# Kernel tuning notes

Hardware: AMD Instinct MI355X
Metric: run time of the kernel (lower is better)

## Reference

```python
import jax, jax.numpy as jnp
import numpy as np
from jax import lax

M = 384   # latent_seq_length (match states); insert states = M+1; K = 2M+1
A = 21    # alphabet_length
B = 64    # batch
L = 256   # max observed sequence length
NEG = -1.0e32  # pyro uses -1/epsilon with epsilon=1e-32 for impossible transitions


def _state_indices(Mloc):
    # state k = m + M*g: match states (g=0) m in 0..M-1, insert states (g=1) m in 0..M
    m_k = np.concatenate([np.arange(Mloc), np.arange(Mloc + 1)]).astype(np.int32)
    g_k = np.concatenate([np.zeros(Mloc, np.int32), np.ones(Mloc + 1, np.int32)])
    s_k = (m_k + 1 - g_k).astype(np.int32)  # next decision position, in 0..M
    return m_k, g_k, s_k


def _arrange(precursor_seq_logits, insert_seq_logits, insert_logits, delete_logits):
    """Profile(M) state arranger: assemble initial/transition/emission logits of the
    MuE profile HMM from insertion (r) and deletion (u) log-simplex params.
    insert_logits[m,j] = [log(1-r_mj), log(r_mj)], same for delete/u. Boundary
    convention r_M=1, u_M=0. Vectorized (gathers + cumsum of the delete chain)
    instead of pyro's dense (M,3,2,K,K) transfer einsum -- same math."""
    Mloc = precursor_seq_logits.shape[0]
    dt = precursor_seq_logits.dtype
    m_k, g_k, s_k = _state_indices(Mloc)
    pad_r = jnp.tile(jnp.array([[[NEG, 0.0]]], dt), (1, 3, 1))  # r_M = 1
    pad_u = jnp.tile(jnp.array([[[0.0, NEG]]], dt), (1, 3, 1))  # u_M = 0
    lre = jnp.concatenate([insert_logits, pad_r], 0)  # (M+1,3,2)
    lue = jnp.concatenate([delete_logits, pad_u], 0)  # (M+1,3,2)
    # delete-chain log prob per skipped position j (enter-and-leave delete, type j=2)
    d2 = insert_logits[:, 2, 0] + delete_logits[:, 2, 1]  # (M,)
    C = jnp.concatenate([jnp.zeros((1,), dt), jnp.cumsum(d2), jnp.zeros((1,), dt)])  # C[j]=sum_{i<j} d2[i]
    # per-source-state factors (K,)
    src_stay = lre[s_k, g_k, 0]   # log(1-r_{s,g})
    src_del = lue[s_k, g_k, 1]    # log u_{s,g}
    src_match = lue[s_k, g_k, 0]  # log(1-u_{s,g})
    src_ins = lre[s_k, g_k, 1]    # log r_{s,g}
    # per-target-state factors (K,)
    t_match = lre[m_k, 2, 0] + lue[m_k, 2, 0]
    t_ins = lre[m_k, 2, 1]
    is_ins = g_k == 1
    t_term = jnp.where(is_ins, t_ins, t_match)
    # transition matrix (K,K): direct step, delete-chain step, or impossible
    chain = (src_stay + src_del - C[s_k + 1])[:, None] + C[m_k][None, :]
    same = m_k[None, :] == s_k[:, None]
    fwdm = m_k[None, :] > s_k[:, None]
    direct = jnp.where(is_ins[None, :], src_ins[:, None], (src_stay + src_match)[:, None])
    trans = jnp.where(same, direct, jnp.where(fwdm, chain + t_term[None, :], NEG))
    # initial vector: virtual source (m=-1, g=0) -> s=0 with j=0 params
    i_direct = jnp.where(is_ins, lre[0, 0, 1], lre[0, 0, 0] + lue[0, 0, 0])
    i_chain = lre[0, 0, 0] + lue[0, 0, 1] - C[1] + C[m_k]
    init = jnp.where(m_k == 0, i_direct, i_chain + t_term)
    # emission logits: match states emit precursor, insert states emit insert_seq
    obs = jnp.concatenate([precursor_seq_logits, insert_seq_logits], 0)  # (K,A)
    return init, trans, obs


def _forward(precursor_seq, insert_seq, insert, delete, seq_data, local_scale):
    # log-softmax normalizations done in ProfileHMM.model
    p = precursor_seq - jax.nn.logsumexp(precursor_seq, -1, keepdims=True)
    iseq = insert_seq - jax.nn.logsumexp(insert_seq, -1, keepdims=True)
    r = insert - jax.nn.logsumexp(insert, -1, keepdims=True)
    u = delete - jax.nn.logsumexp(delete, -1, keepdims=True)
    init, trans, obs = _arrange(p, iseq, r, u)
    # MissingDataDiscreteHMM normalizes all logits
    init = init - jax.nn.logsumexp(init)
    trans = trans - jax.nn.logsumexp(trans, -1, keepdims=True)
    obs = obs - jax.nn.logsumexp(obs, -1, keepdims=True)
    # per-position per-state emission log-prob; all-zero rows (missing) give 0
    vl = jnp.einsum('bla,ka->blk', seq_data, obs)  # (B,L,K)
    alpha = init[None, :] + vl[:, 0]               # (B,K)
    Tprob = jnp.exp(trans)                         # (K,K)

    def step(a, vlt):
        # logsumexp_k(a[b,k] + trans[k,kp]) via stable exp-matmul-log
        mx = jnp.max(a, -1, keepdims=True)
        pr = jnp.exp(a - mx) @ Tprob
        return jnp.log(jnp.maximum(pr, 1e-30)) + mx + vlt, None

    alpha, _ = lax.scan(step, alpha, jnp.moveaxis(vl[:, 1:], 1, 0))
    return local_scale[0] * jax.nn.logsumexp(alpha, -1)  # (B,) scaled log-probs


def setup_inputs() -> dict:
    key = jax.random.key(0)
    ks = jax.random.split(key, 6)
    precursor_seq = jax.random.normal(ks[0], (M, A), jnp.float32)
    insert_seq = jax.random.normal(ks[1], (M + 1, A), jnp.float32)
    indel_prior = jnp.array([10.0, 0.0], jnp.float32)  # indel_prior_bias=10 -> rare indels
    insert = indel_prior + jax.random.normal(ks[2], (M, 3, 2), jnp.float32)
    delete = indel_prior + jax.random.normal(ks[3], (M, 3, 2), jnp.float32)
    lengths = jax.random.randint(ks[4], (B,), L // 2, L + 1)
    letters = jax.random.randint(ks[5], (B, L), 0, A)
    onehot = jax.nn.one_hot(letters, A, dtype=jnp.float32)
    mask = (jnp.arange(L)[None, :] < lengths[:, None]).astype(jnp.float32)
    seq_data = onehot * mask[:, :, None]  # zero rows past length = missing data
    return {"precursor_seq": precursor_seq, "insert_seq": insert_seq,
            "insert": insert, "delete": delete, "seq_data": seq_data,
            "local_scale": jnp.ones((1,), jnp.float32)}


def reference(precursor_seq, insert_seq, insert, delete, seq_data, local_scale):
    return _forward(precursor_seq, insert_seq, insert, delete, seq_data, local_scale)
```

## Files before the change

### kernel.cpp

```cpp
#include <hip/hip_runtime.h>


#define NEGC (-1.0e32f)

typedef float v2f __attribute__((ext_vector_type(2)));

#if __has_builtin(__builtin_elementwise_fma)
#define VFMA(a,b,c) __builtin_elementwise_fma((a),(b),(c))
#else
static __device__ __forceinline__ v2f VFMA(v2f a, v2f b, v2f c) {
    v2f r; r.x = fmaf(a.x,b.x,c.x); r.y = fmaf(a.y,b.y,c.y); return r;
}
#endif
#if __has_builtin(__builtin_elementwise_max)
#define VMAX(a,b) __builtin_elementwise_max((a),(b))
#else
static __device__ __forceinline__ v2f VMAX(v2f a, v2f b) {
    v2f r; r.x = fmaxf(a.x,b.x); r.y = fmaxf(a.y,b.y); return r;
}
#endif
static __device__ __forceinline__ v2f mkv2(float a, float b) { v2f r; r.x = a; r.y = b; return r; }

#if __has_builtin(__builtin_amdgcn_sched_barrier)
#define SCHED_FENCE() __builtin_amdgcn_sched_barrier(0x401)
#else
#define SCHED_FENCE()
#endif

template<int CTRL>
__device__ __forceinline__ float fdpp(float x) {
    union { float f; int i; } u, r;
    u.f = x;
    r.i = __builtin_amdgcn_update_dpp(0, u.i, CTRL, 0xF, 0xF, true);
    return r.f;
}
__device__ __forceinline__ float wsr1(float x) { return fdpp<0x138>(x); }

#define L_TAB   0
#define L_ES    16128
#define L_LETS  16152
#define L_TOTAL 16224

#define S_RN    0
#define S_UN    2304
#define S_EWS   4608
#define S_ETMM  4993
#define S_ETII  5378
#define S_CS    5763
#define S_QA    6148
#define S_D2    6533
#define S_AEM   6917
#define S_AEI   7302
#define S_DMA   7687
#define S_DMB   8072
#define S_DIA   8457
#define S_DIB   8842
#define S_RAW   9227
#define S_RED   9998

struct Buf { v2f em0, em1, em2, ei0, ei1, ei2; float es; };

#define RENORM do { \
    v2f mv_ = VMAX(VMAX(Pm0,Pm1), VMAX(Pm2, VMAX(Pi0, VMAX(Pi1,Pi2)))); \
    float mxr_ = fmaxf(fmaxf(mv_.x, mv_.y), pi384); \
    mxr_ = fmaxf(mxr_, fdpp<0x111>(mxr_)); \
    mxr_ = fmaxf(mxr_, fdpp<0x112>(mxr_)); \
    mxr_ = fmaxf(mxr_, fdpp<0x114>(mxr_)); \
    mxr_ = fmaxf(mxr_, fdpp<0x118>(mxr_)); \
    mxr_ = fmaxf(mxr_, fdpp<0x142>(mxr_)); \
    mxr_ = fmaxf(mxr_, fdpp<0x143>(mxr_)); \
    union { float f; int i; } ub_; ub_.f = mxr_; \
    int bits_ = __builtin_amdgcn_readlane(ub_.i, 63); \
    int E_ = (bits_ >> 23) & 0xff; \
    E_ = (E_ < 71) ? 71 : E_; \
    ksum += 197 - E_; \
    union { int i; float f; } us_; us_.i = (324 - E_) << 23; \
    float sc_ = us_.f; \
    Pm0 *= sc_; Pm1 *= sc_; Pm2 *= sc_; Pi0 *= sc_; Pi1 *= sc_; Pi2 *= sc_; pi384 *= sc_; \
} while (0)

#define FILL(LM, E) do { \
    int lmv_ = (LM); \
    int lmc_ = lmv_ > 20 ? 20 : lmv_; \
    const float* bp_ = smem + lmc_*768 + lane12; \
    float4 q0_ = ((const float4*)bp_)[0], q1_ = ((const float4*)bp_)[1], q2_ = ((const float4*)bp_)[2]; \
    E.em0 = mkv2(q0_.x,q0_.y); E.em1 = mkv2(q0_.z,q0_.w); E.em2 = mkv2(q1_.x,q1_.y); \
    E.ei0 = mkv2(q1_.z,q1_.w); E.ei1 = mkv2(q2_.x,q2_.y); E.ei2 = mkv2(q2_.z,q2_.w); \
    E.es = smem[L_ES + lmv_]; \
} while (0)

#define CORE(CUR, FAST) do { \
    float apx_ = wsr1(Pm2.y); \
    float oldPm_ = Pm2.y; \
    v2f Ap0_ = mkv2(apx_, Pm0.x), Ap1_ = mkv2(Pm0.y, Pm1.x), Ap2_ = mkv2(Pm1.y, Pm2.x); \
    v2f E0_ = VFMA(Pi0, Cei0, Ap0_*Cem0); \
    v2f E1_ = VFMA(Pi1, Cei1, Ap1_*Cem1); \
    v2f E2_ = VFMA(Pi2, Cei2, Ap2_*Cem2); \
    float i0_ = E0_.x; \
    float i1_ = fmaf(w1, i0_, E0_.y); \
    float i2_ = fmaf(w2, i1_, E1_.x); \
    float i3_ = fmaf(w3, i2_, E1_.y); \
    float i4_ = fmaf(w4, i3_, E2_.x); \
    float i5_ = fmaf(w5, i4_, E2_.y); \
    float bb_, bx_; \
    if (FAST) { \
        float u_ = wsr1(i5_); \
        bb_ = fmaf(Ar0, u_, i5_);              \
        bx_ = fmaf(Ar0s, wsr1(u_), u_);        \
    } else { \
        bb_ = i5_; \
        bb_ = fmaf(Ar0, fdpp<0x111>(bb_), bb_); \
        bb_ = fmaf(Ar1, fdpp<0x112>(bb_), bb_); \
        bb_ = fmaf(Ar2, fdpp<0x114>(bb_), bb_); \
        bb_ = fmaf(Ar3, fdpp<0x118>(bb_), bb_); \
        bb_ = fmaf(A15, fdpp<0x142>(bb_), bb_); \
        bb_ = fmaf(A31, fdpp<0x143>(bb_), bb_); \
        bx_ = wsr1(bb_); \
    } \
    v2f Rv0_ = mkv2(bx_, fmaf(pw1, bx_, i0_)); \
    v2f Rv1_ = mkv2(fmaf(pw2, bx_, i1_), fmaf(pw3, bx_, i2_)); \
    v2f Rv2_ = mkv2(fmaf(pw4, bx_, i3_), fmaf(pw5, bx_, i4_)); \
    v2f nm0_ = VFMA(Cgm0, Rv0_, VFMA(Pi0, Cdmb0, Ap0_*Cdma0)); \
    v2f nm1_ = VFMA(Cgm1, Rv1_, VFMA(Pi1, Cdmb1, Ap1_*Cdma1)); \
    v2f nm2_ = VFMA(Cgm2, Rv2_, VFMA(Pi2, Cdmb2, Ap2_*Cdma2)); \
    v2f ni0_ = VFMA(Cgi0, Rv0_, VFMA(Pi0, Cdib0, Ap0_*Cdia0)); \
    v2f ni1_ = VFMA(Cgi1, Rv1_, VFMA(Pi1, Cdib1, Ap1_*Cdia1)); \
    v2f ni2_ = VFMA(Cgi2, Rv2_, VFMA(Pi2, Cdib2, Ap2_*Cdia2)); \
    float np_ = ((oldPm_ + pi384) + bb_) * CUR.es;  \
    Pm0 = nm0_*CUR.em0; Pm1 = nm1_*CUR.em1; Pm2 = nm2_*CUR.em2; \
    Pi0 = ni0_*CUR.ei0; Pi1 = ni1_*CUR.ei1; Pi2 = ni2_*CUR.ei2; \
    pi384 = np_; \
} while (0)

#define ITER(BA,BB,BC,LA,LB,LC,TIDX,FAST) do { \
    FILL(LA, BC); \
    LA = (int)lets[(TIDX)+5]; \
    CORE(BA, FAST); \
    SCHED_FENCE(); \
} while (0)

#define SCANLOOP(FAST) do { \
    for (int it = 0; it < bodies; ++it, t += 12) { \
        ITER(bA,bB,bC,lA,lB,lC,t,FAST); \
        ITER(bB,bC,bA,lB,lC,lA,t+1,FAST); \
        ITER(bC,bA,bB,lC,lA,lB,t+2,FAST); \
        ITER(bA,bB,bC,lA,lB,lC,t+3,FAST); \
        ITER(bB,bC,bA,lB,lC,lA,t+4,FAST); \
        ITER(bC,bA,bB,lC,lA,lB,t+5,FAST); \
        ITER(bA,bB,bC,lA,lB,lC,t+6,FAST); \
        ITER(bB,bC,bA,lB,lC,lA,t+7,FAST); \
        ITER(bC,bA,bB,lC,lA,lB,t+8,FAST); \
        ITER(bA,bB,bC,lA,lB,lC,t+9,FAST); \
        ITER(bB,bC,bA,lB,lC,lA,t+10,FAST); \
        ITER(bC,bA,bB,lC,lA,lB,t+11,FAST); \
        RENORM; \
    } \
    if (rem > 0)  { ITER(bA,bB,bC,lA,lB,lC,t,FAST); ++t; } \
    if (rem > 1)  { ITER(bB,bC,bA,lB,lC,lA,t,FAST); ++t; } \
    if (rem > 2)  { ITER(bC,bA,bB,lC,lA,lB,t,FAST); ++t; } \
    if (rem > 3)  { ITER(bA,bB,bC,lA,lB,lC,t,FAST); ++t; } \
    if (rem > 4)  { ITER(bB,bC,bA,lB,lC,lA,t,FAST); ++t; } \
    if (rem > 5)  { ITER(bC,bA,bB,lC,lA,lB,t,FAST); ++t; } \
    if (rem > 6)  { ITER(bA,bB,bC,lA,lB,lC,t,FAST); ++t; } \
    if (rem > 7)  { ITER(bB,bC,bA,lB,lC,lA,t,FAST); ++t; } \
    if (rem > 8)  { ITER(bC,bA,bB,lC,lA,lB,t,FAST); ++t; } \
    if (rem > 9)  { ITER(bA,bB,bC,lA,lB,lC,t,FAST); ++t; } \
    if (rem > 10) { ITER(bB,bC,bA,lB,lC,lA,t,FAST); ++t; } \
} while (0)

__global__ __launch_bounds__(256, 1) void hmm_fused(
    const float* __restrict__ ps, const float* __restrict__ iseq,
    const float* __restrict__ rr, const float* __restrict__ uu,
    const float* __restrict__ seq, const float* __restrict__ lsc,
    float* __restrict__ out)
{
    __shared__ float smem[L_TOTAL];
    const int tid = threadIdx.x;
    const int lane = tid & 63;
    const int wvid = tid >> 6;
    const int b = blockIdx.x;
    unsigned char* lets = (unsigned char*)(smem + L_LETS);

    float* rn   = smem + S_RN;
    float* un   = smem + S_UN;
    float* ews  = smem + S_EWS;
    float* etmm = smem + S_ETMM;
    float* etii = smem + S_ETII;
    float* Cs   = smem + S_CS;
    float* qa   = smem + S_QA;
    float* d2s  = smem + S_D2;
    float* cAEM = smem + S_AEM;
    float* cAEI = smem + S_AEI;
    float* cDMA = smem + S_DMA;
    float* cDMB = smem + S_DMB;
    float* cDIA = smem + S_DIA;
    float* cDIB = smem + S_DIB;
    float* rawv = smem + S_RAW;
    float* red  = smem + S_RED;

    {
        const float* p = seq + (size_t)b*5376 + tid*21;
        float s = 0.f, wsum = 0.f;
        #pragma unroll
        for (int a = 0; a < 21; ++a) { float v = p[a]; s += v; wsum += v*(float)a; }
        lets[tid] = (s > 0.5f) ? (unsigned char)(int)(wsum + 0.5f) : (unsigned char)21;
        if (tid < 8) lets[256 + tid] = (unsigned char)21;
    }
    for (int row = tid; row < 1152; row += 256) {
        float a = rr[row*2], c = rr[row*2+1];
        float mx = fmaxf(a, c);
        float l = mx + __logf(__expf(a-mx) + __expf(c-mx));
        rn[row*2] = a - l; rn[row*2+1] = c - l;
        a = uu[row*2]; c = uu[row*2+1];
        mx = fmaxf(a, c);
        l = mx + __logf(__expf(a-mx) + __expf(c-mx));
        un[row*2] = a - l; un[row*2+1] = c - l;
    }
    __syncthreads();
    for (int m = tid; m < 384; m += 256) {
        float d = rn[(m*3+2)*2+0] + un[(m*3+2)*2+1];
        d2s[m] = d;
        ews[m] = __expf(d);
        etmm[m] = __expf(rn[(m*3+2)*2+0] + un[(m*3+2)*2+0]);
        etii[m] = __expf(rn[(m*3+2)*2+1]);
    }
    if (tid == 0) { ews[384] = 0.f; etmm[384] = 0.f; etii[384] = 1.f; }
    __syncthreads();
    if (tid < 64) {
        float incl[6]; float z = 0.f;
        #pragma unroll
        for (int i = 0; i < 6; ++i) { z += d2s[lane*6+i]; incl[i] = z; }
        float tot = z;
        #pragma unroll
        for (int d = 1; d < 64; d <<= 1) { float q = __shfl_up(tot, d); if (lane >= d) tot += q; }
        float excl = __shfl_up(tot, 1); if (lane == 0) excl = 0.f;
        #pragma unroll
        for (int i = 0; i < 6; ++i) Cs[lane*6+i+1] = excl + incl[i];
        if (lane == 0) Cs[0] = 0.f;
    } else if (tid < 128) {
        float wv6[6], xv[6], incl[6];
        #pragma unroll
        for (int i = 0; i < 6; ++i) {
            int s = 384 - (lane*6 + i);
            wv6[i] = ews[s]; xv[i] = etii[s] + etmm[s];
        }
        float z = 0.f, Wl = 1.f;
        #pragma unroll
        for (int i = 0; i < 6; ++i) { z = fmaf(wv6[i], z, xv[i]); incl[i] = z; Wl *= wv6[i]; }
        float val = z, wt = Wl;
        #pragma unroll
        for (int d = 1; d < 64; d <<= 1) {
            float pv = __shfl_up(val, d); float pwv = __shfl_up(wt, d);
            if (lane >= d) { val = fmaf(wt, pv, val); wt *= pwv; }
        }
        float excl = __shfl_up(val, 1); if (lane == 0) excl = 0.f;
        float pp = 1.f;
        #pragma unroll
        for (int i = 0; i < 6; ++i) {
            pp *= wv6[i];
            qa[383 - (lane*6 + i)] = fmaf(excl, pp, incl[i]);
        }
        if (lane == 0) qa[384] = 0.f;
    }
    __syncthreads();
    for (int k = tid; k < 769; k += 256) {
        int g = (k < 384) ? 0 : 1;
        int m = (k < 384) ? k : (k - 384);
        int s = m + 1 - g;
        float ss, sd, smv, si;
        if (s <= 383) {
            int base = (s*3 + g)*2;
            ss = rn[base+0]; si = rn[base+1];
            smv = un[base+0]; sd = un[base+1];
        } else { ss = NEGC; si = 0.f; smv = 0.f; sd = NEGC; }
        float d0 = (s <= 383) ? (ss + smv) : NEGC;
        float d1 = si;
        float q = qa[s];
        float lq = (q > 0.f) ? __logf(q) : -1.0e30f;
        float ch = ss + sd + lq;
        float mx = fmaxf(fmaxf(d0, d1), ch);
        float Z = mx + __logf(__expf(d0-mx) + __expf(d1-mx) + __expf(ch-mx));
        float we = __expf(ss + sd - Z);
        float w0 = __expf(d0 - Z);
        float w1v = __expf(d1 - Z);
        if (g == 0) { cAEM[s] = we; cDMA[s] = w0; cDIA[s] = w1v; }
        else        { cAEI[s] = we; cDMB[s] = w0; cDIB[s] = w1v; }
    }
    if (tid == 0) { cAEM[0] = 0.f; cDMA[0] = 0.f; cDIA[0] = 0.f; }
    {
        float r000 = rn[0], r001 = rn[1];
        float u000 = un[0], u001 = un[1];
        for (int k = tid; k < 769; k += 256) {
            int g = (k < 384) ? 0 : 1;
            int m = (k < 384) ? k : (k - 384);
            float v;
            if (m == 0) v = g ? r001 : (r000 + u000);
            else {
                float tt = g ? ((m <= 383) ? rn[(m*3+2)*2+1] : 0.f)
                             : (rn[(m*3+2)*2+0] + un[(m*3+2)*2+0]);
                v = r000 + u001 - Cs[1] + Cs[m] + tt;
            }
            rawv[k] = v;
        }
    }
    __syncthreads();
    {
        float lmax = -3.0e38f;
        for (int k = tid; k < 769; k += 256) lmax = fmaxf(lmax, rawv[k]);
        #pragma unroll
        for (int d = 1; d < 64; d <<= 1) lmax = fmaxf(lmax, __shfl_xor(lmax, d));
        if (lane == 0) red[wvid] = lmax;
    }
    __syncthreads();
    {
        float gmax = fmaxf(fmaxf(red[0], red[1]), fmaxf(red[2], red[3]));
        float lsum = 0.f;
        for (int k = tid; k < 769; k += 256) lsum += __expf(rawv[k] - gmax);
        #pragma unroll
        for (int d = 1; d < 64; d <<= 1) lsum += __shfl_xor(lsum, d);
        if (lane == 0) red[4 + wvid] = lsum;
        __syncthreads();
        float lse = gmax + __logf(red[4] + red[5] + red[6] + red[7]);
        for (int k = tid; k < 769; k += 256) rawv[k] = __expf(rawv[k] - lse);
    }
    __syncthreads();
    const int j0 = lane*6;
    const int lane12 = lane*12;
    v2f Cem0=mkv2(cAEM[j0],cAEM[j0+1]), Cem1=mkv2(cAEM[j0+2],cAEM[j0+3]), Cem2=mkv2(cAEM[j0+4],cAEM[j0+5]);
    v2f Cei0=mkv2(cAEI[j0],cAEI[j0+1]), Cei1=mkv2(cAEI[j0+2],cAEI[j0+3]), Cei2=mkv2(cAEI[j0+4],cAEI[j0+5]);
    v2f Cdma0=mkv2(cDMA[j0],cDMA[j0+1]), Cdma1=mkv2(cDMA[j0+2],cDMA[j0+3]), Cdma2=mkv2(cDMA[j0+4],cDMA[j0+5]);
    v2f Cdmb0=mkv2(cDMB[j0],cDMB[j0+1]), Cdmb1=mkv2(cDMB[j0+2],cDMB[j0+3]), Cdmb2=mkv2(cDMB[j0+4],cDMB[j0+5]);
    v2f Cdia0=mkv2(cDIA[j0],cDIA[j0+1]), Cdia1=mkv2(cDIA[j0+2],cDIA[j0+3]), Cdia2=mkv2(cDIA[j0+4],cDIA[j0+5]);
    v2f Cdib0=mkv2(cDIB[j0],cDIB[j0+1]), Cdib1=mkv2(cDIB[j0+2],cDIB[j0+3]), Cdib2=mkv2(cDIB[j0+4],cDIB[j0+5]);
    v2f Cgm0=mkv2(etmm[j0],etmm[j0+1]), Cgm1=mkv2(etmm[j0+2],etmm[j0+3]), Cgm2=mkv2(etmm[j0+4],etmm[j0+5]);
    v2f Cgi0=mkv2(etii[j0],etii[j0+1]), Cgi1=mkv2(etii[j0+2],etii[j0+3]), Cgi2=mkv2(etii[j0+4],etii[j0+5]);
    v2f Pm0=mkv2(rawv[j0],rawv[j0+1]), Pm1=mkv2(rawv[j0+2],rawv[j0+3]), Pm2=mkv2(rawv[j0+4],rawv[j0+5]);
    v2f Pi0=mkv2(rawv[384+j0],rawv[384+j0+1]), Pi1=mkv2(rawv[384+j0+2],rawv[384+j0+3]), Pi2=mkv2(rawv[384+j0+4],rawv[384+j0+5]);
    float pi384 = rawv[768];
    const float W0=ews[j0], w1=ews[j0+1], w2=ews[j0+2], w3=ews[j0+3], w4=ews[j0+4], w5=ews[j0+5];
    __syncthreads();
    for (int row = tid; row < 769; row += 256) {
        const float* src = (row < 384) ? (ps + row*21) : (iseq + (row-384)*21);
        float mx = -3.0e38f;
        for (int a = 0; a < 21; ++a) mx = fmaxf(mx, src[a]);
        float sm2 = 0.f;
        for (int a = 0; a < 21; ++a) sm2 += __expf(src[a]-mx);
        float inv = 1.0f / sm2;
        if (row < 768) {
            int j = (row < 384) ? row : (row - 384);
            int slot = (j/6)*12 + ((row < 384) ? 0 : 6) + (j%6);
            float* dst = smem + L_TAB + slot;
            for (int a = 0; a < 21; ++a) dst[a*768] = __expf(src[a]-mx)*inv;
        } else {
            for (int a = 0; a < 21; ++a) smem[L_ES + a] = __expf(src[a]-mx)*inv;
            smem[L_ES + 21] = 1.0f; smem[L_ES + 22] = 1.0f; smem[L_ES + 23] = 1.0f;
        }
    }
    __syncthreads();
    if (wvid != 0) return;

    int n = 0;
    #pragma unroll
    for (int c = 0; c < 4; ++c)
        n += __popcll(__ballot(lets[c*64 + lane] != (unsigned char)21));

    const float pw1 = W0, pw2 = pw1*w1, pw3 = pw2*w2, pw4 = pw3*w3, pw5 = pw4*w4;
    const float W = pw5*w5;
    float p_ = W;
    const float Ar0 = p_;
    const float Ar0s = wsr1(Ar0);
    { float q = __shfl_up(p_, 1); p_ *= q; } const float Ar1 = p_;
    { float q = __shfl_up(p_, 2); p_ *= q; } const float Ar2 = p_;
    { float q = __shfl_up(p_, 4); p_ *= q; } const float Ar3 = p_;
    float prefR = W;
    #pragma unroll
    for (int d = 1; d < 16; d <<= 1) { float q = __shfl_up(prefR, d); if ((lane & 15) >= d) prefR *= q; }
    const int rw = lane >> 4;
    const float A15 = (rw == 1 || rw == 3) ? prefR : 0.f;
    const float s47 = __shfl(prefR, 47);
    const float A31 = (rw == 2) ? prefR : ((rw == 3) ? prefR * s47 : 0.f);
    bool bad = (Ar1 != 0.f) || (Ar2 != 0.f) || (Ar3 != 0.f)
             || ((A15 != 0.f) && ((lane & 15) >= 1))
             || ((A31 != 0.f) && (lane >= 33));
    const bool fastAll = (__ballot(bad) == 0ull);

    int ksum = 0;
    {
        int lm0 = (int)lets[0];
        const float* bp = smem + lm0*768 + lane12;
        float4 q0 = ((const float4*)bp)[0], q1 = ((const float4*)bp)[1], q2 = ((const float4*)bp)[2];
        Pm0 *= mkv2(q0.x,q0.y); Pm1 *= mkv2(q0.z,q0.w); Pm2 *= mkv2(q1.x,q1.y);
        Pi0 *= mkv2(q1.z,q1.w); Pi1 *= mkv2(q2.x,q2.y); Pi2 *= mkv2(q2.z,q2.w);
        pi384 *= smem[L_ES + lm0];
        RENORM;
    }

    Buf bA, bB, bC;
    FILL((int)lets[1], bA);
    FILL((int)lets[2], bB);
    int lA = (int)lets[3], lB = (int)lets[4], lC = (int)lets[5];

    const int total = n - 1;
    const int bodies = total / 12;
    const int rem = total - bodies*12;
    int t = 1;
    if (fastAll) SCANLOOP(1);
    else         SCANLOOP(0);

    v2f sv = Pm0 + Pm1 + Pm2 + Pi0 + Pi1 + Pi2;
    float s = sv.x + sv.y + ((lane == 63) ? pi384 : 0.f);
    s += fdpp<0x111>(s); s += fdpp<0x112>(s); s += fdpp<0x114>(s); s += fdpp<0x118>(s);
    s += fdpp<0x142>(s); s += fdpp<0x143>(s);
    if (lane == 63) out[b] = lsc[0] * (__logf(s) - (float)ksum * 0.69314718055994531f);
}

extern "C" void kernel_launch(void* const* d_in, const int* in_sizes, int n_in,
                              void* d_out, int out_size, void* d_ws, size_t ws_size,
                              hipStream_t stream)
{
    const float* ps   = (const float*)d_in[0];
    const float* iseq = (const float*)d_in[1];
    const float* ins  = (const float*)d_in[2];
    const float* del  = (const float*)d_in[3];
    const float* seq  = (const float*)d_in[4];
    const float* lsc  = (const float*)d_in[5];
    float* out = (float*)d_out;
    hmm_fused<<<64, 256, 0, stream>>>(ps, iseq, ins, del, seq, lsc, out);
}
```

Baseline: 106.1 us.

## Pack letter and end-state emission into one word, deepen emission prefetch, interleave pairs

Precomputes a per-step integer that holds the clamped letter index in its low byte and the end-insert emission, truncated, in its upper bits. Each scan step then needs one LDS load for both instead of a letter byte load plus a dependent emission load. The emission buffers rotate over four slots instead of three, so the table fill runs one step further ahead. The packed v2f registers now pair states j and j+3 (table slots permuted to match), so the lane-shift input no longer has to be rebuilt from the previous vectors. The cost is more live registers and a small precision loss in the truncated end-state emission.

```diff
diff --git a/kernel.cpp b/kernel.cpp
--- a/kernel.cpp
+++ b/kernel.cpp
@@ -37,9 +37,8 @@
 __device__ __forceinline__ float wsr1(float x) { return fdpp<0x138>(x); }
 
 #define L_TAB   0
-#define L_ES    16128
-#define L_LETS  16152
-#define L_TOTAL 16224
+#define L_ESL   16128
+#define L_TOTAL 16384
 
 #define S_RN    0
 #define S_UN    2304
@@ -57,11 +56,13 @@
 #define S_DIB   8842
 #define S_RAW   9227
 #define S_RED   9998
+#define S_LETS  10016
+#define S_ES    10082
 
 struct Buf { v2f em0, em1, em2, ei0, ei1, ei2; float es; };
 
 #define RENORM do { \
-    v2f mv_ = VMAX(VMAX(Pm0,Pm1), VMAX(Pm2, VMAX(Pi0, VMAX(Pi1,Pi2)))); \
+    v2f mv_ = VMAX(VMAX(PmA,PmB), VMAX(PmC, VMAX(PiA, VMAX(PiB,PiC)))); \
     float mxr_ = fmaxf(fmaxf(mv_.x, mv_.y), pi384); \
     mxr_ = fmaxf(mxr_, fdpp<0x111>(mxr_)); \
     mxr_ = fmaxf(mxr_, fdpp<0x112>(mxr_)); \
@@ -76,32 +77,31 @@
     ksum += 197 - E_; \
     union { int i; float f; } us_; us_.i = (324 - E_) << 23; \
     float sc_ = us_.f; \
-    Pm0 *= sc_; Pm1 *= sc_; Pm2 *= sc_; Pi0 *= sc_; Pi1 *= sc_; Pi2 *= sc_; pi384 *= sc_; \
+    PmA *= sc_; PmB *= sc_; PmC *= sc_; PiA *= sc_; PiB *= sc_; PiC *= sc_; pi384 *= sc_; \
 } while (0)
 
-#define FILL(LM, E) do { \
-    int lmv_ = (LM); \
-    int lmc_ = lmv_ > 20 ? 20 : lmv_; \
-    const float* bp_ = smem + lmc_*768 + lane12; \
+#define FILLE(E, EV) do { \
+    int lm_ = (EV) & 0xff; \
+    const float* bp_ = smem + lm_*768 + lane12; \
     float4 q0_ = ((const float4*)bp_)[0], q1_ = ((const float4*)bp_)[1], q2_ = ((const float4*)bp_)[2]; \
     E.em0 = mkv2(q0_.x,q0_.y); E.em1 = mkv2(q0_.z,q0_.w); E.em2 = mkv2(q1_.x,q1_.y); \
     E.ei0 = mkv2(q1_.z,q1_.w); E.ei1 = mkv2(q2_.x,q2_.y); E.ei2 = mkv2(q2_.z,q2_.w); \
-    E.es = smem[L_ES + lmv_]; \
+    union { int i; float f; } ue_; ue_.i = (EV) & 0xffffff00; E.es = ue_.f; \
 } while (0)
 
 #define CORE(CUR, FAST) do { \
-    float apx_ = wsr1(Pm2.y); \
-    float oldPm_ = Pm2.y; \
-    v2f Ap0_ = mkv2(apx_, Pm0.x), Ap1_ = mkv2(Pm0.y, Pm1.x), Ap2_ = mkv2(Pm1.y, Pm2.x); \
-    v2f E0_ = VFMA(Pi0, Cei0, Ap0_*Cem0); \
-    v2f E1_ = VFMA(Pi1, Cei1, Ap1_*Cem1); \
-    v2f E2_ = VFMA(Pi2, Cei2, Ap2_*Cem2); \
-    float i0_ = E0_.x; \
-    float i1_ = fmaf(w1, i0_, E0_.y); \
-    float i2_ = fmaf(w2, i1_, E1_.x); \
-    float i3_ = fmaf(w3, i2_, E1_.y); \
-    float i4_ = fmaf(w4, i3_, E2_.x); \
-    float i5_ = fmaf(w5, i4_, E2_.y); \
+    float apx_ = wsr1(PmC.y); \
+    float oldPm_ = PmC.y; \
+    v2f ApA_ = mkv2(apx_, PmC.x); \
+    v2f EA_ = VFMA(PiA, CeiA, ApA_*CemA); \
+    v2f EB_ = VFMA(PiB, CeiB, PmA*CemB); \
+    v2f EC_ = VFMA(PiC, CeiC, PmB*CemC); \
+    float i0_ = EA_.x; \
+    float i1_ = fmaf(w1, i0_, EB_.x); \
+    float i2_ = fmaf(w2, i1_, EC_.x); \
+    float i3_ = fmaf(w3, i2_, EA_.y); \
+    float i4_ = fmaf(w4, i3_, EB_.y); \
+    float i5_ = fmaf(w5, i4_, EC_.y); \
     float bb_, bx_; \
     if (FAST) { \
         float u_ = wsr1(i5_); \
@@ -117,55 +117,50 @@
         bb_ = fmaf(A31, fdpp<0x143>(bb_), bb_); \
         bx_ = wsr1(bb_); \
     } \
-    v2f Rv0_ = mkv2(bx_, fmaf(pw1, bx_, i0_)); \
-    v2f Rv1_ = mkv2(fmaf(pw2, bx_, i1_), fmaf(pw3, bx_, i2_)); \
-    v2f Rv2_ = mkv2(fmaf(pw4, bx_, i3_), fmaf(pw5, bx_, i4_)); \
-    v2f nm0_ = VFMA(Cgm0, Rv0_, VFMA(Pi0, Cdmb0, Ap0_*Cdma0)); \
-    v2f nm1_ = VFMA(Cgm1, Rv1_, VFMA(Pi1, Cdmb1, Ap1_*Cdma1)); \
-    v2f nm2_ = VFMA(Cgm2, Rv2_, VFMA(Pi2, Cdmb2, Ap2_*Cdma2)); \
-    v2f ni0_ = VFMA(Cgi0, Rv0_, VFMA(Pi0, Cdib0, Ap0_*Cdia0)); \
-    v2f ni1_ = VFMA(Cgi1, Rv1_, VFMA(Pi1, Cdib1, Ap1_*Cdia1)); \
-    v2f ni2_ = VFMA(Cgi2, Rv2_, VFMA(Pi2, Cdib2, Ap2_*Cdia2)); \
+    v2f RA_ = mkv2(bx_, fmaf(pw3, bx_, i2_)); \
+    v2f RB_ = mkv2(fmaf(pw1, bx_, i0_), fmaf(pw4, bx_, i3_)); \
+    v2f RC_ = mkv2(fmaf(pw2, bx_, i1_), fmaf(pw5, bx_, i4_)); \
+    v2f nmA_ = VFMA(CgmA, RA_, VFMA(PiA, CdmbA, ApA_*CdmaA)); \
+    v2f nmB_ = VFMA(CgmB, RB_, VFMA(PiB, CdmbB, PmA*CdmaB)); \
+    v2f nmC_ = VFMA(CgmC, RC_, VFMA(PiC, CdmbC, PmB*CdmaC)); \
+    v2f niA_ = VFMA(CgiA, RA_, VFMA(PiA, CdibA, ApA_*CdiaA)); \
+    v2f niB_ = VFMA(CgiB, RB_, VFMA(PiB, CdibB, PmA*CdiaB)); \
+    v2f niC_ = VFMA(CgiC, RC_, VFMA(PiC, CdibC, PmB*CdiaC)); \
     float np_ = ((oldPm_ + pi384) + bb_) * CUR.es;  \
-    Pm0 = nm0_*CUR.em0; Pm1 = nm1_*CUR.em1; Pm2 = nm2_*CUR.em2; \
-    Pi0 = ni0_*CUR.ei0; Pi1 = ni1_*CUR.ei1; Pi2 = ni2_*CUR.ei2; \
+    PmA = nmA_*CUR.em0; PmB = nmB_*CUR.em1; PmC = nmC_*CUR.em2; \
+    PiA = niA_*CUR.ei0; PiB = niB_*CUR.ei1; PiC = niC_*CUR.ei2; \
     pi384 = np_; \
 } while (0)
 
-#define ITER(BA,BB,BC,LA,LB,LC,TIDX,FAST) do { \
-    FILL(LA, BC); \
-    LA = (int)lets[(TIDX)+5]; \
-    CORE(BA, FAST); \
+#define ITER(BU, BF, T, FAST) do { \
+    int ev_ = eU; \
+    FILLE(BF, ev_); \
+    { int ix_ = (T)+4; ix_ = ix_ > 255 ? 255 : ix_; eU = iesl[ix_]; } \
+    CORE(BU, FAST); \
     SCHED_FENCE(); \
 } while (0)
 
 #define SCANLOOP(FAST) do { \
     for (int it = 0; it < bodies; ++it, t += 12) { \
-        ITER(bA,bB,bC,lA,lB,lC,t,FAST); \
-        ITER(bB,bC,bA,lB,lC,lA,t+1,FAST); \
-        ITER(bC,bA,bB,lC,lA,lB,t+2,FAST); \
-        ITER(bA,bB,bC,lA,lB,lC,t+3,FAST); \
-        ITER(bB,bC,bA,lB,lC,lA,t+4,FAST); \
-        ITER(bC,bA,bB,lC,lA,lB,t+5,FAST); \
-        ITER(bA,bB,bC,lA,lB,lC,t+6,FAST); \
-        ITER(bB,bC,bA,lB,lC,lA,t+7,FAST); \
-        ITER(bC,bA,bB,lC,lA,lB,t+8,FAST); \
-        ITER(bA,bB,bC,lA,lB,lC,t+9,FAST); \
-        ITER(bB,bC,bA,lB,lC,lA,t+10,FAST); \
-        ITER(bC,bA,bB,lC,lA,lB,t+11,FAST); \
+        ITER(b1,b0,t,FAST);    ITER(b2,b1,t+1,FAST); \
+        ITER(b3,b2,t+2,FAST);  ITER(b0,b3,t+3,FAST); \
+        ITER(b1,b0,t+4,FAST);  ITER(b2,b1,t+5,FAST); \
+        ITER(b3,b2,t+6,FAST);  ITER(b0,b3,t+7,FAST); \
+        ITER(b1,b0,t+8,FAST);  ITER(b2,b1,t+9,FAST); \
+        ITER(b3,b2,t+10,FAST); ITER(b0,b3,t+11,FAST); \
         RENORM; \
     } \
-    if (rem > 0)  { ITER(bA,bB,bC,lA,lB,lC,t,FAST); ++t; } \
-    if (rem > 1)  { ITER(bB,bC,bA,lB,lC,lA,t,FAST); ++t; } \
-    if (rem > 2)  { ITER(bC,bA,bB,lC,lA,lB,t,FAST); ++t; } \
-    if (rem > 3)  { ITER(bA,bB,bC,lA,lB,lC,t,FAST); ++t; } \
-    if (rem > 4)  { ITER(bB,bC,bA,lB,lC,lA,t,FAST); ++t; } \
-    if (rem > 5)  { ITER(bC,bA,bB,lC,lA,lB,t,FAST); ++t; } \
-    if (rem > 6)  { ITER(bA,bB,bC,lA,lB,lC,t,FAST); ++t; } \
-    if (rem > 7)  { ITER(bB,bC,bA,lB,lC,lA,t,FAST); ++t; } \
-    if (rem > 8)  { ITER(bC,bA,bB,lC,lA,lB,t,FAST); ++t; } \
-    if (rem > 9)  { ITER(bA,bB,bC,lA,lB,lC,t,FAST); ++t; } \
-    if (rem > 10) { ITER(bB,bC,bA,lB,lC,lA,t,FAST); ++t; } \
+    if (rem > 0)  { ITER(b1,b0,t,FAST); ++t; } \
+    if (rem > 1)  { ITER(b2,b1,t,FAST); ++t; } \
+    if (rem > 2)  { ITER(b3,b2,t,FAST); ++t; } \
+    if (rem > 3)  { ITER(b0,b3,t,FAST); ++t; } \
+    if (rem > 4)  { ITER(b1,b0,t,FAST); ++t; } \
+    if (rem > 5)  { ITER(b2,b1,t,FAST); ++t; } \
+    if (rem > 6)  { ITER(b3,b2,t,FAST); ++t; } \
+    if (rem > 7)  { ITER(b0,b3,t,FAST); ++t; } \
+    if (rem > 8)  { ITER(b1,b0,t,FAST); ++t; } \
+    if (rem > 9)  { ITER(b2,b1,t,FAST); ++t; } \
+    if (rem > 10) { ITER(b3,b2,t,FAST); ++t; } \
 } while (0)
 
 __global__ __launch_bounds__(256, 1) void hmm_fused(
@@ -179,7 +174,7 @@
     const int lane = tid & 63;
     const int wvid = tid >> 6;
     const int b = blockIdx.x;
-    unsigned char* lets = (unsigned char*)(smem + L_LETS);
+    unsigned char* lets = (unsigned char*)(smem + S_LETS);
 
     float* rn   = smem + S_RN;
     float* un   = smem + S_UN;
@@ -197,6 +192,7 @@
     float* cDIB = smem + S_DIB;
     float* rawv = smem + S_RAW;
     float* red  = smem + S_RED;
+    float* sES  = smem + S_ES;
 
     {
         const float* p = seq + (size_t)b*5376 + tid*21;
@@ -204,7 +200,6 @@
         #pragma unroll
         for (int a = 0; a < 21; ++a) { float v = p[a]; s += v; wsum += v*(float)a; }
         lets[tid] = (s > 0.5f) ? (unsigned char)(int)(wsum + 0.5f) : (unsigned char)21;
-        if (tid < 8) lets[256 + tid] = (unsigned char)21;
     }
     for (int row = tid; row < 1152; row += 256) {
         float a = rr[row*2], c = rr[row*2+1];
@@ -287,6 +282,15 @@
         else        { cAEI[s] = we; cDMB[s] = w0; cDIB[s] = w1v; }
     }
     if (tid == 0) { cAEM[0] = 0.f; cDMA[0] = 0.f; cDIA[0] = 0.f; }
+    if (tid == 255) {
+        const float* src = iseq + 384*21;
+        float mx = -3.0e38f;
+        for (int a = 0; a < 21; ++a) mx = fmaxf(mx, src[a]);
+        float sm2 = 0.f;
+        for (int a = 0; a < 21; ++a) sm2 += __expf(src[a]-mx);
+        float inv = 1.0f / sm2;
+        for (int a = 0; a < 21; ++a) sES[a] = __expf(src[a]-mx)*inv;
+    }
     {
         float r000 = rn[0], r001 = rn[1];
         float u000 = un[0], u001 = un[1];
@@ -326,43 +330,45 @@
     __syncthreads();
     const int j0 = lane*6;
     const int lane12 = lane*12;
-    v2f Cem0=mkv2(cAEM[j0],cAEM[j0+1]), Cem1=mkv2(cAEM[j0+2],cAEM[j0+3]), Cem2=mkv2(cAEM[j0+4],cAEM[j0+5]);
-    v2f Cei0=mkv2(cAEI[j0],cAEI[j0+1]), Cei1=mkv2(cAEI[j0+2],cAEI[j0+3]), Cei2=mkv2(cAEI[j0+4],cAEI[j0+5]);
-    v2f Cdma0=mkv2(cDMA[j0],cDMA[j0+1]), Cdma1=mkv2(cDMA[j0+2],cDMA[j0+3]), Cdma2=mkv2(cDMA[j0+4],cDMA[j0+5]);
-    v2f Cdmb0=mkv2(cDMB[j0],cDMB[j0+1]), Cdmb1=mkv2(cDMB[j0+2],cDMB[j0+3]), Cdmb2=mkv2(cDMB[j0+4],cDMB[j0+5]);
-    v2f Cdia0=mkv2(cDIA[j0],cDIA[j0+1]), Cdia1=mkv2(cDIA[j0+2],cDIA[j0+3]), Cdia2=mkv2(cDIA[j0+4],cDIA[j0+5]);
-    v2f Cdib0=mkv2(cDIB[j0],cDIB[j0+1]), Cdib1=mkv2(cDIB[j0+2],cDIB[j0+3]), Cdib2=mkv2(cDIB[j0+4],cDIB[j0+5]);
-    v2f Cgm0=mkv2(etmm[j0],etmm[j0+1]), Cgm1=mkv2(etmm[j0+2],etmm[j0+3]), Cgm2=mkv2(etmm[j0+4],etmm[j0+5]);
-    v2f Cgi0=mkv2(etii[j0],etii[j0+1]), Cgi1=mkv2(etii[j0+2],etii[j0+3]), Cgi2=mkv2(etii[j0+4],etii[j0+5]);
-    v2f Pm0=mkv2(rawv[j0],rawv[j0+1]), Pm1=mkv2(rawv[j0+2],rawv[j0+3]), Pm2=mkv2(rawv[j0+4],rawv[j0+5]);
-    v2f Pi0=mkv2(rawv[384+j0],rawv[384+j0+1]), Pi1=mkv2(rawv[384+j0+2],rawv[384+j0+3]), Pi2=mkv2(rawv[384+j0+4],rawv[384+j0+5]);
+    v2f CemA=mkv2(cAEM[j0],cAEM[j0+3]), CemB=mkv2(cAEM[j0+1],cAEM[j0+4]), CemC=mkv2(cAEM[j0+2],cAEM[j0+5]);
+    v2f CeiA=mkv2(cAEI[j0],cAEI[j0+3]), CeiB=mkv2(cAEI[j0+1],cAEI[j0+4]), CeiC=mkv2(cAEI[j0+2],cAEI[j0+5]);
+    v2f CdmaA=mkv2(cDMA[j0],cDMA[j0+3]), CdmaB=mkv2(cDMA[j0+1],cDMA[j0+4]), CdmaC=mkv2(cDMA[j0+2],cDMA[j0+5]);
+    v2f CdmbA=mkv2(cDMB[j0],cDMB[j0+3]), CdmbB=mkv2(cDMB[j0+1],cDMB[j0+4]), CdmbC=mkv2(cDMB[j0+2],cDMB[j0+5]);
+    v2f CdiaA=mkv2(cDIA[j0],cDIA[j0+3]), CdiaB=mkv2(cDIA[j0+1],cDIA[j0+4]), CdiaC=mkv2(cDIA[j0+2],cDIA[j0+5]);
+    v2f CdibA=mkv2(cDIB[j0],cDIB[j0+3]), CdibB=mkv2(cDIB[j0+1],cDIB[j0+4]), CdibC=mkv2(cDIB[j0+2],cDIB[j0+5]);
+    v2f CgmA=mkv2(etmm[j0],etmm[j0+3]), CgmB=mkv2(etmm[j0+1],etmm[j0+4]), CgmC=mkv2(etmm[j0+2],etmm[j0+5]);
+    v2f CgiA=mkv2(etii[j0],etii[j0+3]), CgiB=mkv2(etii[j0+1],etii[j0+4]), CgiC=mkv2(etii[j0+2],etii[j0+5]);
+    v2f PmA=mkv2(rawv[j0],rawv[j0+3]), PmB=mkv2(rawv[j0+1],rawv[j0+4]), PmC=mkv2(rawv[j0+2],rawv[j0+5]);
+    v2f PiA=mkv2(rawv[384+j0],rawv[384+j0+3]), PiB=mkv2(rawv[384+j0+1],rawv[384+j0+4]), PiC=mkv2(rawv[384+j0+2],rawv[384+j0+5]);
     float pi384 = rawv[768];
     const float W0=ews[j0], w1=ews[j0+1], w2=ews[j0+2], w3=ews[j0+3], w4=ews[j0+4], w5=ews[j0+5];
-    __syncthreads();
-    for (int row = tid; row < 769; row += 256) {
+    {
+        int l = (int)lets[tid]; l = (l > 20) ? 20 : l;
+        union { float f; int i; } u; u.f = sES[l];
+        ((int*)smem)[L_ESL + tid] = (u.i & 0xffffff00) | l;
+    }
+    int n = 0;
+    #pragma unroll
+    for (int c = 0; c < 4; ++c)
+        n += __popcll(__ballot(lets[c*64 + lane] != (unsigned char)21));
+    __syncthreads();
+    for (int row = tid; row < 768; row += 256) {
         const float* src = (row < 384) ? (ps + row*21) : (iseq + (row-384)*21);
         float mx = -3.0e38f;
         for (int a = 0; a < 21; ++a) mx = fmaxf(mx, src[a]);
         float sm2 = 0.f;
         for (int a = 0; a < 21; ++a) sm2 += __expf(src[a]-mx);
         float inv = 1.0f / sm2;
-        if (row < 768) {
-            int j = (row < 384) ? row : (row - 384);
-            int slot = (j/6)*12 + ((row < 384) ? 0 : 6) + (j%6);
-            float* dst = smem + L_TAB + slot;
-            for (int a = 0; a < 21; ++a) dst[a*768] = __expf(src[a]-mx)*inv;
-        } else {
-            for (int a = 0; a < 21; ++a) smem[L_ES + a] = __expf(src[a]-mx)*inv;
-            smem[L_ES + 21] = 1.0f; smem[L_ES + 22] = 1.0f; smem[L_ES + 23] = 1.0f;
-        }
+        int j = (row < 384) ? row : (row - 384);
+        int k = j % 6;
+        int slot = (j/6)*12 + ((row < 384) ? 0 : 6) + (k%3)*2 + (k/3);
+        float* dst = smem + L_TAB + slot;
+        for (int a = 0; a < 21; ++a) dst[a*768] = __expf(src[a]-mx)*inv;
     }
     __syncthreads();
     if (wvid != 0) return;
 
-    int n = 0;
-    #pragma unroll
-    for (int c = 0; c < 4; ++c)
-        n += __popcll(__ballot(lets[c*64 + lane] != (unsigned char)21));
+    const int* iesl = ((const int*)smem) + L_ESL;
 
     const float pw1 = W0, pw2 = pw1*w1, pw3 = pw2*w2, pw4 = pw3*w3, pw5 = pw4*w4;
     const float W = pw5*w5;
@@ -386,19 +392,22 @@
 
     int ksum = 0;
     {
-        int lm0 = (int)lets[0];
+        int e0 = iesl[0];
+        int lm0 = e0 & 0xff;
         const float* bp = smem + lm0*768 + lane12;
         float4 q0 = ((const float4*)bp)[0], q1 = ((const float4*)bp)[1], q2 = ((const float4*)bp)[2];
-        Pm0 *= mkv2(q0.x,q0.y); Pm1 *= mkv2(q0.z,q0.w); Pm2 *= mkv2(q1.x,q1.y);
-        Pi0 *= mkv2(q1.z,q1.w); Pi1 *= mkv2(q2.x,q2.y); Pi2 *= mkv2(q2.z,q2.w);
-        pi384 *= smem[L_ES + lm0];
+        PmA *= mkv2(q0.x,q0.y); PmB *= mkv2(q0.z,q0.w); PmC *= mkv2(q1.x,q1.y);
+        PiA *= mkv2(q1.z,q1.w); PiB *= mkv2(q2.x,q2.y); PiC *= mkv2(q2.z,q2.w);
+        union { int i; float f; } u0; u0.i = e0 & 0xffffff00;
+        pi384 *= u0.f;
         RENORM;
     }
 
-    Buf bA, bB, bC;
-    FILL((int)lets[1], bA);
-    FILL((int)lets[2], bB);
-    int lA = (int)lets[3], lB = (int)lets[4], lC = (int)lets[5];
+    Buf b0, b1, b2, b3;
+    { int e = iesl[1]; FILLE(b1, e); }
+    { int e = iesl[2]; FILLE(b2, e); }
+    { int e = iesl[3]; FILLE(b3, e); }
+    int eU = iesl[4];
 
     const int total = n - 1;
     const int bodies = total / 12;
@@ -407,7 +416,7 @@
     if (fastAll) SCANLOOP(1);
     else         SCANLOOP(0);
 
-    v2f sv = Pm0 + Pm1 + Pm2 + Pi0 + Pi1 + Pi2;
+    v2f sv = PmA + PmB + PmC + PiA + PiB + PiC;
     float s = sv.x + sv.y + ((lane == 63) ? pi384 : 0.f);
     s += fdpp<0x111>(s); s += fdpp<0x112>(s); s += fdpp<0x114>(s); s += fdpp<0x118>(s);
     s += fdpp<0x142>(s); s += fdpp<0x143>(s);
```

Result: no change. 105.0 us (-1.1%).
